# Performance work log

Hardware: AMD Instinct MI355X
Metric: run time of the kernel (lower is better)

Reference implementation:

```python
import jax, jax.numpy as jnp
import numpy as np

S, K, O = 8192, 1024, 4096  # seq_len, in_features, out_features


def setup_inputs() -> dict:
    key = jax.random.key(0)
    k1, k2, k3, k4, k5 = jax.random.split(key, 5)
    x = jax.random.randint(k1, (S, K), -128, 128, dtype=jnp.int8)
    weight_q = jax.random.randint(k2, (O, K), -128, 128, dtype=jnp.int8)
    scale_x = jax.random.uniform(k3, (), jnp.float32, 0.01, 0.1)
    scale_w = jax.random.uniform(k4, (), jnp.float32, 0.01, 0.1)
    scale_y = jax.random.uniform(k5, (S,), jnp.float32, 0.5, 2.0)  # per-row output scale
    return {"x": x, "weight_q": weight_q, "scale_x": scale_x,
            "scale_w": scale_w, "scale_y": scale_y}


def reference(x, weight_q, scale_x, scale_w, scale_y):
    # int8 GEMM with int32 accumulation: [S,K] @ [O,K]^T -> [S,O]
    acc = jnp.einsum('sk,ok->so', x.astype(jnp.int32), weight_q.astype(jnp.int32))
    # fused per-row requantization: scale_y[:seq_len] gives per-row scale
    requant_scale = (scale_x * scale_w / scale_y).astype(jnp.float32)  # [S]
    scaled = acc.astype(jnp.float32) * requant_scale[:, None]
    out_q = jnp.clip(jnp.round(scaled), -128.0, 127.0).astype(jnp.int8)
    return out_q, scale_y
```

## Files before the change

kernel.cpp:

```cpp
#include <hip/hip_runtime.h>


#define S_DIM 8192
#define K_DIM 1024
#define O_DIM 4096
#define BM 128
#define BN 128
#define BK 64
#define NITER (K_DIM / BK)
#define TILE_BYTES (BM * BK)

using i32x4 = __attribute__((ext_vector_type(4))) int;

__device__ __forceinline__ void load_lds16(const void* g, void* l) {
  __builtin_amdgcn_global_load_lds(
      (const __attribute__((address_space(1))) void*)g,
      (__attribute__((address_space(3))) void*)l, 16, 0, 0);
}

__global__ void pack_kernel(const int* __restrict__ xi, const int* __restrict__ wi,
                            const float* __restrict__ sy,
                            uint4* __restrict__ ap, uint4* __restrict__ bp,
                            float* __restrict__ out_sy) {
  const int tid = blockIdx.x * blockDim.x + threadIdx.x;
  const int nA = S_DIM * K_DIM / 16;
  const int nB = O_DIM * K_DIM / 16;

  const int* src;
  uint4* dst;
  int j;
  if (tid < nA) {
    src = xi; dst = ap; j = tid;
  } else if (tid < nA + nB) {
    src = wi; dst = bp; j = tid - nA;
  } else {
    return;
  }
  const int t = j >> 9;
  const int idx = j & 511;
  const int r = idx >> 2;
  const int cs = idx & 3;
  const int c = cs ^ (r & 3);
  const int band = t >> 4;
  const int kt = t & 15;
  const int row = band * 128 + r;
  const int4* s4 = (const int4*)src + row * 256 + kt * 16 + c * 4;
  int4 v0 = s4[0], v1 = s4[1], v2 = s4[2], v3 = s4[3];
  uint4 o;
  o.x = (v0.x & 0xff) | ((v0.y & 0xff) << 8) | ((v0.z & 0xff) << 16) | (((unsigned)v0.w & 0xff) << 24);
  o.y = (v1.x & 0xff) | ((v1.y & 0xff) << 8) | ((v1.z & 0xff) << 16) | (((unsigned)v1.w & 0xff) << 24);
  o.z = (v2.x & 0xff) | ((v2.y & 0xff) << 8) | ((v2.z & 0xff) << 16) | (((unsigned)v2.w & 0xff) << 24);
  o.w = (v3.x & 0xff) | ((v3.y & 0xff) << 8) | ((v3.z & 0xff) << 16) | (((unsigned)v3.w & 0xff) << 24);
  dst[j] = o;
  if (tid < S_DIM) out_sy[tid] = sy[tid];
}

__global__ __launch_bounds__(256, 3) void gemm_i8_kernel(
    const signed char* __restrict__ Ap,
    const signed char* __restrict__ Bp,
    const float* __restrict__ sx, const float* __restrict__ sw,
    const float* __restrict__ sy, float* __restrict__ out) {
  __shared__ __align__(16) signed char As[3][TILE_BYTES];
  __shared__ __align__(16) signed char Bs[3][TILE_BYTES];

  const int tid = threadIdx.x;
  const int wave = tid >> 6;
  const int lane = tid & 63;
  const int wm = wave >> 1;
  const int wn = wave & 1;
  const int rowBase = blockIdx.x * BM;
  const int colBase = blockIdx.y * BN;

  const int soff = wave * 1024 + lane * 16;
  const signed char* gA = Ap + (size_t)blockIdx.x * NITER * TILE_BYTES + soff;
  const signed char* gB = Bp + (size_t)blockIdx.y * NITER * TILE_BYTES + soff;
  signed char* ldsA = (signed char*)As + wave * 1024;
  signed char* ldsB = (signed char*)Bs + wave * 1024;

  i32x4 acc[4][4] = {};

  const int fr = lane & 15;
  const int fq = (((lane >> 4) ^ (fr & 3)) & 3) * 16;

  load_lds16(gA, ldsA);
  load_lds16(gA + 4096, ldsA + 4096);
  load_lds16(gB, ldsB);
  load_lds16(gB + 4096, ldsB + 4096);
  asm volatile("" ::: "memory");
  load_lds16(gA + TILE_BYTES, ldsA + TILE_BYTES);
  load_lds16(gA + TILE_BYTES + 4096, ldsA + TILE_BYTES + 4096);
  load_lds16(gB + TILE_BYTES, ldsB + TILE_BYTES);
  load_lds16(gB + TILE_BYTES + 4096, ldsB + TILE_BYTES + 4096);

#pragma unroll
  for (int it = 0; it < NITER; ++it) {
    if (it + 1 < NITER) {
      asm volatile("s_waitcnt vmcnt(4) lgkmcnt(0)" ::: "memory");
    } else {
      asm volatile("s_waitcnt vmcnt(0) lgkmcnt(0)" ::: "memory");
    }
    __builtin_amdgcn_s_barrier();
    asm volatile("" ::: "memory");

    if (it + 2 < NITER) {
      const int boff = ((it + 2) % 3) * TILE_BYTES;
      const size_t goff = (size_t)(it + 2) * TILE_BYTES;
      load_lds16(gA + goff, ldsA + boff);
      load_lds16(gA + goff + 4096, ldsA + boff + 4096);
      load_lds16(gB + goff, ldsB + boff);
      load_lds16(gB + goff + 4096, ldsB + boff + 4096);
    }

    const signed char* curA = As[it % 3];
    const signed char* curB = Bs[it % 3];
    i32x4 bf[4];
#pragma unroll
    for (int ni = 0; ni < 4; ++ni)
      bf[ni] = *(const i32x4*)(curB + (wn * 64 + ni * 16 + fr) * BK + fq);

#pragma unroll
    for (int mi = 0; mi < 4; ++mi) {
      i32x4 af = *(const i32x4*)(curA + (wm * 64 + mi * 16 + fr) * BK + fq);
#pragma unroll
      for (int ni = 0; ni < 4; ++ni)
        acc[mi][ni] =
            __builtin_amdgcn_mfma_i32_16x16x64_i8(af, bf[ni], acc[mi][ni], 0, 0, 0);
    }
  }

  const float sxw = sx[0] * sw[0];
  const int quad = lane >> 4;
#pragma unroll
  for (int mi = 0; mi < 4; ++mi) {
#pragma unroll
    for (int r = 0; r < 4; ++r) {
      const int s = rowBase + wm * 64 + mi * 16 + quad * 4 + r;
      const float rs = sxw / sy[s];
      float* orow = out + (size_t)s * O_DIM + colBase + wn * 64 + fr;
#pragma unroll
      for (int ni = 0; ni < 4; ++ni) {
        float f = rintf((float)acc[mi][ni][r] * rs);
        f = fminf(127.0f, fmaxf(-128.0f, f));
        orow[ni * 16] = f;
      }
    }
  }
}

extern "C" void kernel_launch(void* const* d_in, const int* in_sizes, int n_in,
                              void* d_out, int out_size, void* d_ws, size_t ws_size,
                              hipStream_t stream) {
  const int* x = (const int*)d_in[0];
  const int* w = (const int*)d_in[1];
  const float* sx = (const float*)d_in[2];
  const float* sw = (const float*)d_in[3];
  const float* sy = (const float*)d_in[4];
  float* out = (float*)d_out;

  uint4* ap = (uint4*)d_ws;
  uint4* bp = ap + (size_t)S_DIM * K_DIM / 16;

  const int total = S_DIM * K_DIM / 16 + O_DIM * K_DIM / 16;
  pack_kernel<<<(total + 255) / 256, 256, 0, stream>>>(
      x, w, sy, ap, bp, out + (size_t)S_DIM * O_DIM);

  dim3 grid(S_DIM / BM, O_DIM / BN);
  gemm_i8_kernel<<<grid, 256, 0, stream>>>(
      (const signed char*)ap, (const signed char*)bp, sx, sw, sy, out);
}
```

Baseline: 220.5 us.

## Double GEMM block rows to 256 with 8 waves sharing each B tile

Each block now covers 256 output rows instead of 128. It uses 512 threads (8 waves) and loads two packed 128-row A bands plus one B band per K step. Every loaded B tile is therefore reused across twice as many rows, cutting global and LDS traffic for B per output, and the grid has half as many blocks. In exchange LDS per block rises to 72KB and registers are shared by more waves, which may lower occupancy.

```diff
diff --git a/kernel.cpp b/kernel.cpp
--- a/kernel.cpp
+++ b/kernel.cpp
@@ -4,11 +4,13 @@
 #define S_DIM 8192
 #define K_DIM 1024
 #define O_DIM 4096
-#define BM 128
+#define BM 256
 #define BN 128
 #define BK 64
 #define NITER (K_DIM / BK)
-#define TILE_BYTES (BM * BK)
+#define TILE_BYTES (128 * BK)
+#define A_SLOT (2 * TILE_BYTES)
+#define B_SLOT TILE_BYTES
 
 using i32x4 = __attribute__((ext_vector_type(4))) int;
 
@@ -55,13 +57,13 @@
   if (tid < S_DIM) out_sy[tid] = sy[tid];
 }
 
-__global__ __launch_bounds__(256, 3) void gemm_i8_kernel(
+__global__ __launch_bounds__(512, 4) void gemm_i8_kernel(
     const signed char* __restrict__ Ap,
     const signed char* __restrict__ Bp,
     const float* __restrict__ sx, const float* __restrict__ sw,
     const float* __restrict__ sy, float* __restrict__ out) {
-  __shared__ __align__(16) signed char As[3][TILE_BYTES];
-  __shared__ __align__(16) signed char Bs[3][TILE_BYTES];
+  __shared__ __align__(16) signed char As[3][A_SLOT];
+  __shared__ __align__(16) signed char Bs[3][B_SLOT];
 
   const int tid = threadIdx.x;
   const int wave = tid >> 6;
@@ -72,30 +74,32 @@
   const int colBase = blockIdx.y * BN;
 
   const int soff = wave * 1024 + lane * 16;
-  const signed char* gA = Ap + (size_t)blockIdx.x * NITER * TILE_BYTES + soff;
-  const signed char* gB = Bp + (size_t)blockIdx.y * NITER * TILE_BYTES + soff;
-  signed char* ldsA = (signed char*)As + wave * 1024;
-  signed char* ldsB = (signed char*)Bs + wave * 1024;
+  const signed char* gA0 = Ap + (size_t)(2 * blockIdx.x) * NITER * TILE_BYTES + soff;
+  const signed char* gA1 = Ap + (size_t)(2 * blockIdx.x + 1) * NITER * TILE_BYTES + soff;
+  const signed char* gB  = Bp + (size_t)blockIdx.y * NITER * TILE_BYTES + soff;
+  signed char* ldsA = (signed char*)As + soff;
+  signed char* ldsB = (signed char*)Bs + soff;
 
   i32x4 acc[4][4] = {};
 
   const int fr = lane & 15;
   const int fq = (((lane >> 4) ^ (fr & 3)) & 3) * 16;
 
-  load_lds16(gA, ldsA);
-  load_lds16(gA + 4096, ldsA + 4096);
+  load_lds16(gA0, ldsA);
+  load_lds16(gA1, ldsA + TILE_BYTES);
   load_lds16(gB, ldsB);
-  load_lds16(gB + 4096, ldsB + 4096);
   asm volatile("" ::: "memory");
-  load_lds16(gA + TILE_BYTES, ldsA + TILE_BYTES);
-  load_lds16(gA + TILE_BYTES + 4096, ldsA + TILE_BYTES + 4096);
-  load_lds16(gB + TILE_BYTES, ldsB + TILE_BYTES);
-  load_lds16(gB + TILE_BYTES + 4096, ldsB + TILE_BYTES + 4096);
+  {
+    const size_t goff = TILE_BYTES;
+    load_lds16(gA0 + goff, ldsA + A_SLOT);
+    load_lds16(gA1 + goff, ldsA + A_SLOT + TILE_BYTES);
+    load_lds16(gB + goff, ldsB + B_SLOT);
+  }
 
 #pragma unroll
   for (int it = 0; it < NITER; ++it) {
     if (it + 1 < NITER) {
-      asm volatile("s_waitcnt vmcnt(4) lgkmcnt(0)" ::: "memory");
+      asm volatile("s_waitcnt vmcnt(3) lgkmcnt(0)" ::: "memory");
     } else {
       asm volatile("s_waitcnt vmcnt(0) lgkmcnt(0)" ::: "memory");
     }
@@ -103,12 +107,11 @@
     asm volatile("" ::: "memory");
 
     if (it + 2 < NITER) {
-      const int boff = ((it + 2) % 3) * TILE_BYTES;
+      const int slot = (it + 2) % 3;
       const size_t goff = (size_t)(it + 2) * TILE_BYTES;
-      load_lds16(gA + goff, ldsA + boff);
-      load_lds16(gA + goff + 4096, ldsA + boff + 4096);
-      load_lds16(gB + goff, ldsB + boff);
-      load_lds16(gB + goff + 4096, ldsB + boff + 4096);
+      load_lds16(gA0 + goff, ldsA + slot * A_SLOT);
+      load_lds16(gA1 + goff, ldsA + slot * A_SLOT + TILE_BYTES);
+      load_lds16(gB + goff, ldsB + slot * B_SLOT);
     }
 
     const signed char* curA = As[it % 3];
@@ -165,6 +168,6 @@
       x, w, sy, ap, bp, out + (size_t)S_DIM * O_DIM);
 
   dim3 grid(S_DIM / BM, O_DIM / BN);
-  gemm_i8_kernel<<<grid, 256, 0, stream>>>(
+  gemm_i8_kernel<<<grid, 512, 0, stream>>>(
       (const signed char*)ap, (const signed char*)bp, sx, sw, sy, out);
 }
```

After: 199.6 us. 1.1x faster.
